# Optimization experiments

Hardware: AMD Instinct MI355X
Metric: run time of the kernel (lower is better)

## Reference

```python
import jax, jax.numpy as jnp
import numpy as np

IN_FEATURES = 2048
OUT_FEATURES = 8192


def ternary_quantize(w):
    # BitNet 1.58b: scale = mean(|w|), round to {-1,0,1}, rescale
    scale = jnp.mean(jnp.abs(w)) + 1e-8
    w_q = jnp.clip(jnp.round(w / scale), -1.0, 1.0)
    return w_q * scale


def setup_inputs() -> dict:
    key = jax.random.key(0)
    kx, kw = jax.random.split(key)
    x = jax.random.normal(kx, (4, 2048, IN_FEATURES), dtype=jnp.float32)
    # nn.init.normal_(std=1/sqrt(in_features))
    weight = jax.random.normal(kw, (OUT_FEATURES, IN_FEATURES), dtype=jnp.float32) / np.sqrt(IN_FEATURES)
    return {"x": x, "weight": weight}


def reference(x, weight):
    w = ternary_quantize(weight)
    # F.linear: x @ w.T  -> [B, S, out_features]
    return jnp.einsum('bsd,od->bso', x, w)
```

## Files before the change

### kernel.cpp

```cpp
#include <hip/hip_runtime.h>
#include <hip/hip_bf16.h>
#include <stdint.h>


typedef __attribute__((ext_vector_type(8))) short   s16x8;
typedef __attribute__((ext_vector_type(4))) float   f32x4;

#define K_DIM   2048
#define K2      4096
#define N_DIM   8192
#define N4      4194304

__global__ void k_abs_part(const float4* __restrict__ w4, float* __restrict__ part) {
    int tid = blockIdx.x * 256 + threadIdx.x;
    float s = 0.f;
    for (int i = tid; i < N4; i += gridDim.x * 256) {
        float4 v = w4[i];
        s += fabsf(v.x) + fabsf(v.y) + fabsf(v.z) + fabsf(v.w);
    }
    for (int off = 32; off > 0; off >>= 1) s += __shfl_down(s, off, 64);
    __shared__ float tmp[4];
    int lane = threadIdx.x & 63, wid = threadIdx.x >> 6;
    if (lane == 0) tmp[wid] = s;
    __syncthreads();
    if (threadIdx.x == 0) part[blockIdx.x] = tmp[0] + tmp[1] + tmp[2] + tmp[3];
}

__global__ void k_abs_final(const float* __restrict__ part, float* __restrict__ scale) {
    float s = part[threadIdx.x] + part[threadIdx.x + 256] +
              part[threadIdx.x + 512] + part[threadIdx.x + 768];
    for (int off = 32; off > 0; off >>= 1) s += __shfl_down(s, off, 64);
    __shared__ float tmp[4];
    int lane = threadIdx.x & 63, wid = threadIdx.x >> 6;
    if (lane == 0) tmp[wid] = s;
    __syncthreads();
    if (threadIdx.x == 0) scale[0] = (tmp[0] + tmp[1] + tmp[2] + tmp[3]) / 16777216.0f + 1e-8f;
}

__device__ __forceinline__ uint32_t f2b(float f) {
    uint32_t u = __builtin_bit_cast(uint32_t, f);
    return (u + 0x7FFFu + ((u >> 16) & 1u)) >> 16;
}

__global__ void k_prep(const float4* __restrict__ w4, const float4* __restrict__ x4,
                       const float* __restrict__ scale_p,
                       uint2* __restrict__ wq, uint2* __restrict__ xb) {
    int tid = (blockIdx.x & 2047) * 256 + threadIdx.x;
    if (blockIdx.x < 2048) {
        const float sc = *scale_p;
        for (int i = tid; i < N4; i += 2048 * 256) {
            float4 v = w4[i];
            float q0 = rintf(v.x / sc), q1 = rintf(v.y / sc);
            float q2 = rintf(v.z / sc), q3 = rintf(v.w / sc);
            uint32_t b0 = (q0 == 0.f) ? 0u : (q0 > 0.f ? 0x3F80u : 0xBF80u);
            uint32_t b1 = (q1 == 0.f) ? 0u : (q1 > 0.f ? 0x3F80u : 0xBF80u);
            uint32_t b2 = (q2 == 0.f) ? 0u : (q2 > 0.f ? 0x3F80u : 0xBF80u);
            uint32_t b3 = (q3 == 0.f) ? 0u : (q3 > 0.f ? 0x3F80u : 0xBF80u);
            uint2 o; o.x = b0 | (b1 << 16); o.y = b2 | (b3 << 16);
            wq[i] = o;
        }
    } else {
        for (int i = tid; i < N4; i += 2048 * 256) {
            float4 v = x4[i];
            uint2 o;
            o.x = f2b(v.x) | (f2b(v.y) << 16);
            o.y = f2b(v.z) | (f2b(v.w) << 16);
            xb[i] = o;
        }
    }
}

__device__ __forceinline__ void mfma16(f32x4& c, s16x8 a, s16x8 b) {
    asm("v_mfma_f32_16x16x32_bf16 %0, %1, %2, %0" : "+v"(c) : "v"(a), "v"(b));
}
__device__ __forceinline__ void load_lds16(const void* g, void* l) {
    __builtin_amdgcn_global_load_lds(
        (const __attribute__((address_space(1))) uint32_t*)g,
        (__attribute__((address_space(3))) uint32_t*)l, 16, 0, 0);
}

#define SBAR __builtin_amdgcn_s_barrier()
#define WAIT_VM(N) asm volatile("s_waitcnt vmcnt(" #N ")" ::: "memory")

#define C0 0
#define C1 65536

__global__ __launch_bounds__(512, 2) void k_gemm(
    const unsigned short* __restrict__ Xb,
    const unsigned short* __restrict__ Wb,
    const float* __restrict__ scale_p,
    float* __restrict__ out)
{
    extern __shared__ uint8_t smem[];
    const int tid  = threadIdx.x;
    const int lane = tid & 63;
    const int wid  = tid >> 6;
    const int wr   = wid >> 2;
    const int wc   = wid & 3;

    const int bid = blockIdx.x;
    const int xcd = bid & 7;
    const int l   = bid >> 3;
    const int tileRow = xcd * 4 + ((l >> 3) & 3);
    const int tileCol = (l >> 5) * 8 + (l & 7);

    const uint8_t* gA = (const uint8_t*)Xb + (size_t)tileRow * 256 * K2;
    const uint8_t* gB = (const uint8_t*)Wb + (size_t)tileCol * 256 * K2;

    const int srow = tid >> 3, sslot = tid & 7;
    const size_t srcOff = (size_t)srow * K2 + (size_t)((sslot ^ (srow & 7)) * 16);
    const uint8_t* gAs = gA + srcOff;
    const uint8_t* gBs = gB + srcOff;
    const int dstOff = tid * 16;

    const int rA = wr * 128 + (lane & 15);
    const int rB = wc * 64  + (lane & 15);
    const int h  = lane >> 4;
    const int pA0 = rA * 128 + (((h    ) ^ (rA & 7)) * 16);
    const int pA1 = rA * 128 + (((4 + h) ^ (rA & 7)) * 16);
    const int pB0 = rB * 128 + (((h    ) ^ (rB & 7)) * 16);
    const int pB1 = rB * 128 + (((4 + h) ^ (rB & 7)) * 16);

    s16x8 a[8][2], b[4][2];
    f32x4 acc[8][4];
    #pragma unroll
    for (int m = 0; m < 8; ++m)
        #pragma unroll
        for (int n = 0; n < 4; ++n) acc[m][n] = (f32x4){0.f, 0.f, 0.f, 0.f};

#define LD8(OFF) (*(const s16x8*)(smem + (OFF)))
#define STAGE(LBASE, GP, BOFF) do { \
    load_lds16((GP) + (BOFF),          smem + (LBASE) + dstOff); \
    load_lds16((GP) + (BOFF) + 262144, smem + (LBASE) + 8192 + dstOff); } while (0)

#define RD_A03(AB) do { _Pragma("unroll") for (int m = 0; m < 4; ++m) { \
    a[m][0] = LD8((AB) + pA0 + m * 2048); a[m][1] = LD8((AB) + pA1 + m * 2048); } } while (0)
#define RD_A47(AB) do { _Pragma("unroll") for (int m = 4; m < 8; ++m) { \
    a[m][0] = LD8((AB) + pA0 + m * 2048); a[m][1] = LD8((AB) + pA1 + m * 2048); } } while (0)
#define RD_B01(AB) do { _Pragma("unroll") for (int n = 0; n < 2; ++n) { \
    b[n][0] = LD8((AB) + 32768 + pB0 + n * 2048); b[n][1] = LD8((AB) + 32768 + pB1 + n * 2048); } } while (0)
#define RD_B23(AB) do { _Pragma("unroll") for (int n = 2; n < 4; ++n) { \
    b[n][0] = LD8((AB) + 32768 + pB0 + n * 2048); b[n][1] = LD8((AB) + 32768 + pB1 + n * 2048); } } while (0)

#define MFMA_Q(MLO, NLO) do { \
    __builtin_amdgcn_s_setprio(1); \
    _Pragma("unroll") for (int kk = 0; kk < 2; ++kk) \
        _Pragma("unroll") for (int m = 0; m < 4; ++m) \
            _Pragma("unroll") for (int n = 0; n < 2; ++n) \
                mfma16(acc[(MLO) + m][(NLO) + n], a[(MLO) + m][kk], b[(NLO) + n][kk]); \
    __builtin_amdgcn_s_setprio(0); } while (0)

    STAGE(C0,         gAs, 0);   STAGE(C0 + 16384, gAs, 524288);
    STAGE(C0 + 32768, gBs, 0);   STAGE(C0 + 49152, gBs, 524288);
    STAGE(C1,         gAs, 128); STAGE(C1 + 16384, gAs, 524288 + 128);
    STAGE(C1 + 32768, gBs, 128); STAGE(C1 + 49152, gBs, 524288 + 128);
    WAIT_VM(8);
    SBAR;

    #pragma unroll 1
    for (int i = 0; i < 15; ++i) {
        const int kb1 = (2 * i + 1) * 128;
        const int kb2 = kb1 + 128;
        const int kb3 = kb1 + 256;
        STAGE(C1 + 32768, gBs, kb1);
        RD_A03(C0); RD_B01(C0);
        MFMA_Q(0, 0);
        STAGE(C1 + 49152, gBs, 524288 + kb1);
        RD_A47(C0);
        MFMA_Q(4, 0);
        SBAR;
        STAGE(C0, gAs, kb2);
        RD_B23(C0);
        MFMA_Q(0, 2);
        STAGE(C0 + 16384, gAs, 524288 + kb2);
        MFMA_Q(4, 2);
        WAIT_VM(4); SBAR;
        STAGE(C0 + 32768, gBs, kb2);
        RD_A03(C1); RD_B01(C1);
        MFMA_Q(0, 0);
        STAGE(C0 + 49152, gBs, 524288 + kb2);
        RD_A47(C1);
        MFMA_Q(4, 0);
        SBAR;
        STAGE(C1, gAs, kb3);
        RD_B23(C1);
        MFMA_Q(0, 2);
        STAGE(C1 + 16384, gAs, 524288 + kb3);
        MFMA_Q(4, 2);
        WAIT_VM(4); SBAR;
    }

    {
        const int kb1 = 31 * 128;
        STAGE(C1 + 32768, gBs, kb1);
        RD_A03(C0); RD_B01(C0);
        MFMA_Q(0, 0);
        STAGE(C1 + 49152, gBs, 524288 + kb1);
        RD_A47(C0);
        MFMA_Q(4, 0);
        SBAR;
        RD_B23(C0);
        MFMA_Q(0, 2);
        MFMA_Q(4, 2);
        WAIT_VM(0); SBAR;
        RD_A03(C1); RD_B01(C1);
        MFMA_Q(0, 0);
        RD_A47(C1);
        MFMA_Q(4, 0);
        RD_B23(C1);
        MFMA_Q(0, 2);
        MFMA_Q(4, 2);
    }

    const float sc = *scale_p;
    const int orow0 = tileRow * 256 + wr * 128 + ((lane >> 4) << 2);
    const int ocol0 = tileCol * 256 + wc * 64 + (lane & 15);
    #pragma unroll
    for (int m = 0; m < 8; ++m)
        #pragma unroll
        for (int n = 0; n < 4; ++n)
            #pragma unroll
            for (int j = 0; j < 4; ++j)
                out[(size_t)(orow0 + m * 16 + j) * N_DIM + (ocol0 + n * 16)] = acc[m][n][j] * sc;

#undef LD8
#undef STAGE
#undef RD_A03
#undef RD_A47
#undef RD_B01
#undef RD_B23
#undef MFMA_Q
}

extern "C" void kernel_launch(void* const* d_in, const int* in_sizes, int n_in,
                              void* d_out, int out_size, void* d_ws, size_t ws_size,
                              hipStream_t stream) {
    const float* x = (const float*)d_in[0];
    const float* w = (const float*)d_in[1];
    float* out = (float*)d_out;
    uint8_t* ws = (uint8_t*)d_ws;

    float* part  = (float*)ws;
    float* scale = (float*)(ws + 4096);
    unsigned short* Xb = (unsigned short*)(ws + 8192);
    unsigned short* Wb = (unsigned short*)(ws + 8192 + 33554432ull);

    (void)hipFuncSetAttribute((const void*)k_gemm,
                              hipFuncAttributeMaxDynamicSharedMemorySize, 131072);

    hipLaunchKernelGGL(k_abs_part, dim3(1024), dim3(256), 0, stream, (const float4*)w, part);
    hipLaunchKernelGGL(k_abs_final, dim3(1), dim3(256), 0, stream, part, scale);
    hipLaunchKernelGGL(k_prep, dim3(4096), dim3(256), 0, stream,
                       (const float4*)w, (const float4*)x, scale, (uint2*)Wb, (uint2*)Xb);
    hipLaunchKernelGGL(k_gemm, dim3(1024), dim3(512), 131072, stream, Xb, Wb, scale, out);
}
```

Before: 277.2 us.

## Load GEMM B operand directly from global into registers, halve LDS

The weight (B) operand is no longer staged through LDS. Each wave now reads its own B fragments straight from global memory into registers, one k-step ahead, while the activation (A) operand keeps its double-buffered LDS staging. This halves the dynamic LDS per block to 64KB, which should let two blocks share a CU and removes the B LDS writes, reads and bank traffic. In exchange, waves that share the same columns load the same B data redundantly, each lane reads 16B chunks from rows that are far apart in memory, and global-load latency is now exposed inside the MFMA schedule with hand-tuned vmcnt waits.

```diff
diff --git a/kernel.cpp b/kernel.cpp
--- a/kernel.cpp
+++ b/kernel.cpp
@@ -83,7 +83,7 @@
 #define WAIT_VM(N) asm volatile("s_waitcnt vmcnt(" #N ")" ::: "memory")
 
 #define C0 0
-#define C1 65536
+#define C1 32768
 
 __global__ __launch_bounds__(512, 2) void k_gemm(
     const unsigned short* __restrict__ Xb,
@@ -105,21 +105,19 @@
     const int tileCol = (l >> 5) * 8 + (l & 7);
 
     const uint8_t* gA = (const uint8_t*)Xb + (size_t)tileRow * 256 * K2;
-    const uint8_t* gB = (const uint8_t*)Wb + (size_t)tileCol * 256 * K2;
 
     const int srow = tid >> 3, sslot = tid & 7;
     const size_t srcOff = (size_t)srow * K2 + (size_t)((sslot ^ (srow & 7)) * 16);
     const uint8_t* gAs = gA + srcOff;
-    const uint8_t* gBs = gB + srcOff;
     const int dstOff = tid * 16;
 
     const int rA = wr * 128 + (lane & 15);
-    const int rB = wc * 64  + (lane & 15);
     const int h  = lane >> 4;
     const int pA0 = rA * 128 + (((h    ) ^ (rA & 7)) * 16);
     const int pA1 = rA * 128 + (((4 + h) ^ (rA & 7)) * 16);
-    const int pB0 = rB * 128 + (((h    ) ^ (rB & 7)) * 16);
-    const int pB1 = rB * 128 + (((4 + h) ^ (rB & 7)) * 16);
+
+    const uint8_t* gBl = (const uint8_t*)Wb +
+        ((size_t)tileCol * 256 + (size_t)(wc * 64 + (lane & 15))) * K2 + (size_t)(h * 16);
 
     s16x8 a[8][2], b[4][2];
     f32x4 acc[8][4];
@@ -137,10 +135,13 @@
     a[m][0] = LD8((AB) + pA0 + m * 2048); a[m][1] = LD8((AB) + pA1 + m * 2048); } } while (0)
 #define RD_A47(AB) do { _Pragma("unroll") for (int m = 4; m < 8; ++m) { \
     a[m][0] = LD8((AB) + pA0 + m * 2048); a[m][1] = LD8((AB) + pA1 + m * 2048); } } while (0)
-#define RD_B01(AB) do { _Pragma("unroll") for (int n = 0; n < 2; ++n) { \
-    b[n][0] = LD8((AB) + 32768 + pB0 + n * 2048); b[n][1] = LD8((AB) + 32768 + pB1 + n * 2048); } } while (0)
-#define RD_B23(AB) do { _Pragma("unroll") for (int n = 2; n < 4; ++n) { \
-    b[n][0] = LD8((AB) + 32768 + pB0 + n * 2048); b[n][1] = LD8((AB) + 32768 + pB1 + n * 2048); } } while (0)
+
+#define GLB_B01(KT) do { _Pragma("unroll") for (int n = 0; n < 2; ++n) \
+    _Pragma("unroll") for (int kk = 0; kk < 2; ++kk) \
+        b[n][kk] = *(const s16x8*)(gBl + (size_t)n * 65536 + (size_t)(KT) * 128 + kk * 64); } while (0)
+#define GLB_B23(KT) do { _Pragma("unroll") for (int n = 2; n < 4; ++n) \
+    _Pragma("unroll") for (int kk = 0; kk < 2; ++kk) \
+        b[n][kk] = *(const s16x8*)(gBl + (size_t)n * 65536 + (size_t)(KT) * 128 + kk * 64); } while (0)
 
 #define MFMA_Q(MLO, NLO) do { \
     __builtin_amdgcn_s_setprio(1); \
@@ -150,64 +151,57 @@
                 mfma16(acc[(MLO) + m][(NLO) + n], a[(MLO) + m][kk], b[(NLO) + n][kk]); \
     __builtin_amdgcn_s_setprio(0); } while (0)
 
-    STAGE(C0,         gAs, 0);   STAGE(C0 + 16384, gAs, 524288);
-    STAGE(C0 + 32768, gBs, 0);   STAGE(C0 + 49152, gBs, 524288);
-    STAGE(C1,         gAs, 128); STAGE(C1 + 16384, gAs, 524288 + 128);
-    STAGE(C1 + 32768, gBs, 128); STAGE(C1 + 49152, gBs, 524288 + 128);
+    STAGE(C0,        gAs, 0);   STAGE(C0 + 16384, gAs, 524288);
+    GLB_B01(0);
+    STAGE(C1,        gAs, 128); STAGE(C1 + 16384, gAs, 524288 + 128);
     WAIT_VM(8);
     SBAR;
 
     #pragma unroll 1
     for (int i = 0; i < 15; ++i) {
-        const int kb1 = (2 * i + 1) * 128;
-        const int kb2 = kb1 + 128;
-        const int kb3 = kb1 + 256;
-        STAGE(C1 + 32768, gBs, kb1);
-        RD_A03(C0); RD_B01(C0);
-        MFMA_Q(0, 0);
-        STAGE(C1 + 49152, gBs, 524288 + kb1);
+        const int t0 = 2 * i, t1 = 2 * i + 1;
+        GLB_B23(t0);
+        RD_A03(C0);
+        MFMA_Q(0, 0);
         RD_A47(C0);
         MFMA_Q(4, 0);
         SBAR;
-        STAGE(C0, gAs, kb2);
-        RD_B23(C0);
-        MFMA_Q(0, 2);
-        STAGE(C0 + 16384, gAs, 524288 + kb2);
-        MFMA_Q(4, 2);
-        WAIT_VM(4); SBAR;
-        STAGE(C0 + 32768, gBs, kb2);
-        RD_A03(C1); RD_B01(C1);
-        MFMA_Q(0, 0);
-        STAGE(C0 + 49152, gBs, 524288 + kb2);
+        GLB_B01(t0 + 1);
+        STAGE(C0, gAs, (t0 + 2) * 128);
+        MFMA_Q(0, 2);
+        STAGE(C0 + 16384, gAs, 524288 + (t0 + 2) * 128);
+        MFMA_Q(4, 2);
+        WAIT_VM(12); SBAR;
+        GLB_B23(t1);
+        RD_A03(C1);
+        MFMA_Q(0, 0);
         RD_A47(C1);
         MFMA_Q(4, 0);
         SBAR;
-        STAGE(C1, gAs, kb3);
-        RD_B23(C1);
-        MFMA_Q(0, 2);
-        STAGE(C1 + 16384, gAs, 524288 + kb3);
-        MFMA_Q(4, 2);
-        WAIT_VM(4); SBAR;
+        GLB_B01(t1 + 1);
+        STAGE(C1, gAs, (t1 + 2) * 128);
+        MFMA_Q(0, 2);
+        STAGE(C1 + 16384, gAs, 524288 + (t1 + 2) * 128);
+        MFMA_Q(4, 2);
+        WAIT_VM(12); SBAR;
     }
 
     {
-        const int kb1 = 31 * 128;
-        STAGE(C1 + 32768, gBs, kb1);
-        RD_A03(C0); RD_B01(C0);
-        MFMA_Q(0, 0);
-        STAGE(C1 + 49152, gBs, 524288 + kb1);
+        GLB_B23(30);
+        RD_A03(C0);
+        MFMA_Q(0, 0);
         RD_A47(C0);
         MFMA_Q(4, 0);
         SBAR;
-        RD_B23(C0);
-        MFMA_Q(0, 2);
-        MFMA_Q(4, 2);
-        WAIT_VM(0); SBAR;
-        RD_A03(C1); RD_B01(C1);
+        GLB_B01(31);
+        MFMA_Q(0, 2);
+        MFMA_Q(4, 2);
+        WAIT_VM(8); SBAR;
+        GLB_B23(31);
+        RD_A03(C1);
         MFMA_Q(0, 0);
         RD_A47(C1);
         MFMA_Q(4, 0);
-        RD_B23(C1);
         MFMA_Q(0, 2);
         MFMA_Q(4, 2);
     }
@@ -227,8 +221,8 @@
 #undef STAGE
 #undef RD_A03
 #undef RD_A47
-#undef RD_B01
-#undef RD_B23
+#undef GLB_B01
+#undef GLB_B23
 #undef MFMA_Q
 }
 
@@ -246,11 +240,11 @@
     unsigned short* Wb = (unsigned short*)(ws + 8192 + 33554432ull);
 
     (void)hipFuncSetAttribute((const void*)k_gemm,
-                              hipFuncAttributeMaxDynamicSharedMemorySize, 131072);
+                              hipFuncAttributeMaxDynamicSharedMemorySize, 65536);
 
     hipLaunchKernelGGL(k_abs_part, dim3(1024), dim3(256), 0, stream, (const float4*)w, part);
     hipLaunchKernelGGL(k_abs_final, dim3(1), dim3(256), 0, stream, part, scale);
     hipLaunchKernelGGL(k_prep, dim3(4096), dim3(256), 0, stream,
                        (const float4*)w, (const float4*)x, scale, (uint2*)Wb, (uint2*)Xb);
-    hipLaunchKernelGGL(k_gemm, dim3(1024), dim3(512), 131072, stream, Xb, Wb, scale, out);
-}
+    hipLaunchKernelGGL(k_gemm, dim3(1024), dim3(512), 65536, stream, Xb, Wb, scale, out);
+}
```

Result: slower. 420.4 us (+51.6%).
